# Kernel optimization log

Measured on AMD Instinct MI355X. Metric: run time of the kernel, lower is better.

Reference implementation:

```python
import jax, jax.numpy as jnp
import numpy as np

N = 8192        # nodes
IN_DIM = 512
OUT_DIM = 512
NUM_HEADS = 1   # required for view(-1,3)/view(-1,1,1) consistency in original code
K_NEIGH = 16


def setup_inputs() -> dict:
    key = jax.random.key(0)
    k0, k1, k2, k3, k4 = jax.random.split(key, 5)
    s = 1.0 / np.sqrt(IN_DIM)
    h = jax.random.normal(k0, (N, IN_DIM), dtype=jnp.float32)
    # nn.Linear default init: U(-1/sqrt(fan_in), 1/sqrt(fan_in)), bias=False
    Wq = jax.random.uniform(k1, (OUT_DIM * NUM_HEADS, IN_DIM), jnp.float32, -s, s)
    Wk = jax.random.uniform(k2, (OUT_DIM * NUM_HEADS, IN_DIM), jnp.float32, -s, s)
    Wv = jax.random.uniform(k3, (OUT_DIM * NUM_HEADS, IN_DIM), jnp.float32, -s, s)
    Wg = jax.random.uniform(k4, (3 * NUM_HEADS, IN_DIM), jnp.float32, -s, s)
    return {"h": h, "Wq": Wq, "Wk": Wk, "Wv": Wv, "Wg": Wg}


def _knn_edges(coords, k):
    # dgl.knn_graph semantics: each node receives edges from its k nearest
    # points (self included). src = neighbor, dst = query node.
    sq = jnp.sum(coords * coords, axis=-1)                      # [N]
    neg_d2 = 2.0 * (coords @ coords.T) - sq[:, None] - sq[None, :]  # -||xi-xj||^2, [N,N]
    _, idx = jax.lax.top_k(neg_d2, k)                           # [N,k] nearest per row
    n = coords.shape[0]
    src = idx.reshape(-1)                                       # [N*k]
    dst = jnp.repeat(jnp.arange(n, dtype=idx.dtype), k)         # [N*k]
    return src, dst


def reference(h, Wq, Wk, Wv, Wg):
    n = h.shape[0]
    D = OUT_DIM
    scale = jnp.float32(np.sqrt(D))

    Q_h = (h @ Wq.T).reshape(n, NUM_HEADS, D)
    K_h = (h @ Wk.T).reshape(n, NUM_HEADS, D)
    V_h = (h @ Wv.T).reshape(n, NUM_HEADS, D)
    G_h = (h @ Wg.T).reshape(n, NUM_HEADS, 3)

    coords = G_h.reshape(n, 3)  # num_heads == 1
    src, dst = _knn_edges(coords, K_NEIGH)  # E = n * K_NEIGH edges

    # edge-wise attention score: exp(clip((K_src . Q_dst)/sqrt(D), -5, 5))
    score = jnp.sum(K_h[src] * Q_h[dst], axis=-1, keepdims=True)     # [E,1,1]
    score_e = jnp.exp(jnp.clip(score / scale, -5.0, 5.0))

    # distance decay: exp(clip(-||G_src - G_dst|| / sqrt(D), -5, 5))
    dist = -jnp.sqrt(jnp.sum((G_h[src] - G_h[dst]) ** 2, axis=-1) + 1e-6)  # [E,1]
    distance = jnp.exp(jnp.clip(dist / scale, -5.0, 5.0))

    weight = score_e.reshape(-1, 1, 1) * distance.reshape(-1, 1, 1)  # [E,1,1]
    v1 = weight * V_h[src]                                           # [E,1,D]

    wV = jax.ops.segment_sum(v1, dst, num_segments=n)                # [n,1,D]
    z = jax.ops.segment_sum(score_e, dst, num_segments=n)            # [n,1,1]
    z = jnp.broadcast_to(z.reshape(n, 1, 1), (n, 1, D))

    mask = z > 0
    out = jnp.where(mask, wV / jnp.where(mask, z, 1.0), wV)
    return out
```

## Files before the change

### kernel.cpp

```cpp
#include <hip/hip_runtime.h>
#include <hip/hip_bf16.h>
#include <math.h>

#define N_NODES 8192
#define IN_DIM  512
#define OUT_DIM 512
#define KN      16
#define CAP     128
#define QPB     8

typedef __attribute__((ext_vector_type(8))) short bf16x8;
typedef __attribute__((ext_vector_type(4))) float f32x4;

__device__ __forceinline__ ushort f2bf(float x) {
  __hip_bfloat16 b = __float2bfloat16(x);
  return *reinterpret_cast<ushort*>(&b);
}
__device__ __forceinline__ float bflo(unsigned u) { return __uint_as_float(u << 16); }
__device__ __forceinline__ float bfhi(unsigned u) { return __uint_as_float(u & 0xffff0000u); }

#define GLOAD_LDS16(gp, lp)                                                     \
  __builtin_amdgcn_global_load_lds((const __attribute__((address_space(1))) void*)(gp), \
                                   (__attribute__((address_space(3))) void*)(lp), 16, 0, 0)

__global__ __launch_bounds__(256) void prep_split(
    const float* __restrict__ h, const float* __restrict__ Wg,
    const float* __restrict__ Wq, const float* __restrict__ Wk,
    const float* __restrict__ Wv,
    ushort* __restrict__ A2, ushort* __restrict__ Bqk, ushort* __restrict__ Bv,
    double* __restrict__ Gx, double* __restrict__ Gy,
    double* __restrict__ Gz, double* __restrict__ Gsq,
    float4* __restrict__ gpk) {
  if (blockIdx.x < 2048) {
    const int node = (blockIdx.x * 256 + threadIdx.x) >> 6;
    const int lane = threadIdx.x & 63;
    const int k = lane * 8;
    const float* hr = h + (size_t)node * IN_DIM;

    float4 v0 = *(const float4*)&hr[k];
    float4 v1 = *(const float4*)&hr[k + 4];

    ushort h0 = f2bf(v0.x), h1 = f2bf(v0.y), h2 = f2bf(v0.z), h3 = f2bf(v0.w);
    ushort h4 = f2bf(v1.x), h5 = f2bf(v1.y), h6 = f2bf(v1.z), h7 = f2bf(v1.w);
    ushort4 hiA = make_ushort4(h0, h1, h2, h3);
    ushort4 hiB = make_ushort4(h4, h5, h6, h7);
    ushort4 loA = make_ushort4(f2bf(v0.x - bflo((unsigned)h0)), f2bf(v0.y - bflo((unsigned)h1)),
                               f2bf(v0.z - bflo((unsigned)h2)), f2bf(v0.w - bflo((unsigned)h3)));
    ushort4 loB = make_ushort4(f2bf(v1.x - bflo((unsigned)h4)), f2bf(v1.y - bflo((unsigned)h5)),
                               f2bf(v1.z - bflo((unsigned)h6)), f2bf(v1.w - bflo((unsigned)h7)));
    size_t base = (size_t)node * 1024 + k;
    *(ushort4*)&A2[base]           = hiA;
    *(ushort4*)&A2[base + 4]       = hiB;
    *(ushort4*)&A2[base + 512]     = loA;
    *(ushort4*)&A2[base + 512 + 4] = loB;

    float4 w0a = *(const float4*)&Wg[0 * IN_DIM + k];
    float4 w0b = *(const float4*)&Wg[0 * IN_DIM + k + 4];
    float4 w1a = *(const float4*)&Wg[1 * IN_DIM + k];
    float4 w1b = *(const float4*)&Wg[1 * IN_DIM + k + 4];
    float4 w2a = *(const float4*)&Wg[2 * IN_DIM + k];
    float4 w2b = *(const float4*)&Wg[2 * IN_DIM + k + 4];

    double s0 = 0.0, s1 = 0.0, s2 = 0.0;
    s0 += (double)v0.x * w0a.x; s0 += (double)v0.y * w0a.y;
    s0 += (double)v0.z * w0a.z; s0 += (double)v0.w * w0a.w;
    s0 += (double)v1.x * w0b.x; s0 += (double)v1.y * w0b.y;
    s0 += (double)v1.z * w0b.z; s0 += (double)v1.w * w0b.w;
    s1 += (double)v0.x * w1a.x; s1 += (double)v0.y * w1a.y;
    s1 += (double)v0.z * w1a.z; s1 += (double)v0.w * w1a.w;
    s1 += (double)v1.x * w1b.x; s1 += (double)v1.y * w1b.y;
    s1 += (double)v1.z * w1b.z; s1 += (double)v1.w * w1b.w;
    s2 += (double)v0.x * w2a.x; s2 += (double)v0.y * w2a.y;
    s2 += (double)v0.z * w2a.z; s2 += (double)v0.w * w2a.w;
    s2 += (double)v1.x * w2b.x; s2 += (double)v1.y * w2b.y;
    s2 += (double)v1.z * w2b.z; s2 += (double)v1.w * w2b.w;

    #pragma unroll
    for (int off = 32; off; off >>= 1) {
      s0 += __shfl_down(s0, off);
      s1 += __shfl_down(s1, off);
      s2 += __shfl_down(s2, off);
    }
    if (lane == 0) {
      double sq = s0 * s0 + s1 * s1 + s2 * s2;
      Gx[node] = s0; Gy[node] = s1; Gz[node] = s2; Gsq[node] = sq;
      gpk[node] = make_float4((float)s0, (float)s1, (float)s2, -(float)sq);
    }
  } else {
    int i = (blockIdx.x - 2048) * 256 + threadIdx.x;
    int n  = i >> 7;
    int kc = (i & 127) << 2;
    if (n < 1024) {
      const float* W = (n < 512) ? Wq : Wk;
      int r = n & 511;
      float4 v = *(const float4*)&W[(size_t)r * 512 + kc];
      *(ushort4*)&Bqk[(size_t)n * 512 + kc] =
          make_ushort4(f2bf(v.x), f2bf(v.y), f2bf(v.z), f2bf(v.w));
    } else {
      int r = n - 1024;
      float4 v = *(const float4*)&Wv[(size_t)r * 512 + kc];
      ushort4 hv = make_ushort4(f2bf(v.x), f2bf(v.y), f2bf(v.z), f2bf(v.w));
      *(ushort4*)&Bv[(size_t)r * 1024 + kc]       = hv;
      *(ushort4*)&Bv[(size_t)r * 1024 + 512 + kc] = hv;
    }
  }
}

__global__ __launch_bounds__(256) void gemm_qkv(
    const ushort* __restrict__ A2, const ushort* __restrict__ Bqk,
    const ushort* __restrict__ Bv,
    ushort* __restrict__ Q2, ushort* __restrict__ K2, ushort* __restrict__ V2) {
  __shared__ ushort lA[128 * 32];
  __shared__ ushort lB[128 * 32];
  const int tid = threadIdx.x, w = tid >> 6, lane = tid & 63;
  const int id = blockIdx.x;
  const int sw = (id & 7) * 96 + (id >> 3);
  const int bm = sw / 12, bn = sw % 12;
  const int wr = w >> 1, wc = w & 1;
  const bool isv = (bn >= 8);
  const int  kmax = isv ? 1024 : 512;
  const int  ldb  = isv ? 1024 : 512;
  const ushort* Bb = isv ? (Bv + (size_t)(bn - 8) * 128 * 1024)
                         : (Bqk + (size_t)bn * 128 * 512);

  f32x4 acc[4][4] = {};

  const int   srow = w * 32 + (lane >> 2);
  const int   scol = (lane & 3) * 8;
  const size_t gA0 = (size_t)(bm * 128 + srow) * 1024 + scol;
  const size_t gB0 = (size_t)srow * ldb + scol;

  for (int k0 = 0; k0 < kmax; k0 += 32) {
    GLOAD_LDS16(&A2[gA0 + k0],                    &lA[w * 1024]);
    GLOAD_LDS16(&A2[gA0 + 16 * 1024 + k0],        &lA[w * 1024 + 512]);
    GLOAD_LDS16(&Bb[gB0 + k0],                    &lB[w * 1024]);
    GLOAD_LDS16(&Bb[gB0 + (size_t)16 * ldb + k0], &lB[w * 1024 + 512]);
    __syncthreads();

    const int ar = wr * 64 + (lane & 15);
    const int br = wc * 64 + (lane & 15);
    const int kc = (lane >> 4) * 8;
    bf16x8 af[4], bfr[4];
    #pragma unroll
    for (int f = 0; f < 4; ++f) {
      af[f]  = *(const bf16x8*)&lA[(ar + f * 16) * 32 + kc];
      bfr[f] = *(const bf16x8*)&lB[(br + f * 16) * 32 + kc];
    }
    #pragma unroll
    for (int fm = 0; fm < 4; ++fm)
      #pragma unroll
      for (int fn = 0; fn < 4; ++fn)
        acc[fm][fn] = __builtin_amdgcn_mfma_f32_16x16x32_bf16(af[fm], bfr[fn], acc[fm][fn], 0, 0, 0);
    __syncthreads();
  }

  ushort* Cm = isv ? V2 : (bn < 4 ? Q2 : K2);
  const int col  = (isv ? (bn - 8) : (bn & 3)) * 128 + wc * 64 + (lane & 15);
  const int row0 = bm * 128 + wr * 64 + (lane >> 4) * 4;
  #pragma unroll
  for (int fm = 0; fm < 4; ++fm)
    #pragma unroll
    for (int fn = 0; fn < 4; ++fn)
      #pragma unroll
      for (int r = 0; r < 4; ++r)
        Cm[(size_t)(row0 + fm * 16 + r) * 512 + col + fn * 16] = f2bf(acc[fm][fn][r]);
}

__global__ __launch_bounds__(256) void knn_kernel(
    const float4* __restrict__ gpk,
    const double* __restrict__ Gx, const double* __restrict__ Gy,
    const double* __restrict__ Gz, const double* __restrict__ Gsq,
    int* __restrict__ knn) {
  const int tid   = threadIdx.x;
  const int w     = tid >> 6;
  const int lane  = tid & 63;
  const int qbase = blockIdx.x * QPB;

  __shared__ float  s_tmax[QPB][256];
  __shared__ int    s_cand[QPB][CAP];
  __shared__ double s_dval[QPB][CAP];
  __shared__ int    s_cnt[QPB];
  __shared__ float  s_T[QPB];

  float q2x[QPB], q2y[QPB], q2z[QPB], tmax[QPB];
  #pragma unroll
  for (int s = 0; s < QPB; ++s) {
    float4 qv = gpk[qbase + s];
    q2x[s] = 2.f * qv.x; q2y[s] = 2.f * qv.y; q2z[s] = 2.f * qv.z;
    tmax[s] = -1e30f;
  }
  if (tid < QPB) s_cnt[tid] = 0;

  {
    float4 c0 = gpk[tid];
    float4 c1 = gpk[tid + 256];
    for (int i = 0; i < 16; ++i) {
      int nx = ((i + 1) & 15) * 512;
      float4 n0 = gpk[tid + nx];
      float4 n1 = gpk[tid + nx + 256];
      #pragma unroll
      for (int s = 0; s < QPB; ++s) {
        float v0 = fmaf(q2x[s], c0.x, fmaf(q2y[s], c0.y, fmaf(q2z[s], c0.z, c0.w)));
        float v1 = fmaf(q2x[s], c1.x, fmaf(q2y[s], c1.y, fmaf(q2z[s], c1.z, c1.w)));
        tmax[s] = fmaxf(fmaxf(tmax[s], v0), v1);
      }
      c0 = n0; c1 = n1;
    }
  }
  #pragma unroll
  for (int s = 0; s < QPB; ++s) s_tmax[s][tid] = tmax[s];
  __syncthreads();

  #pragma unroll
  for (int qq = 0; qq < 2; ++qq) {
    int q = w * 2 + qq;
    float v = fmaxf(fmaxf(s_tmax[q][lane], s_tmax[q][lane + 64]),
                    fmaxf(s_tmax[q][lane + 128], s_tmax[q][lane + 192]));
    unsigned b = __float_as_uint(v);
    unsigned u = b ^ ((unsigned)((int)b >> 31) | 0x80000000u);
    unsigned thr = 0;
    for (int bit = 31; bit >= 0; --bit) {
      unsigned cand = thr | (1u << bit);
      unsigned long long m = __ballot(u >= cand);
      if (__popcll(m) >= KN) thr = cand;
    }
    unsigned tb = (thr & 0x80000000u) ? (thr ^ 0x80000000u) : ~thr;
    if (lane == 0) s_T[q] = __uint_as_float(tb);
  }
  __syncthreads();

  float Ts[QPB];
  #pragma unroll
  for (int s = 0; s < QPB; ++s) Ts[s] = s_T[s];
  {
    float4 c0 = gpk[tid];
    float4 c1 = gpk[tid + 256];
    for (int i = 0; i < 16; ++i) {
      int nx = ((i + 1) & 15) * 512;
      float4 n0 = gpk[tid + nx];
      float4 n1 = gpk[tid + nx + 256];
      int j0 = tid + i * 512, j1 = j0 + 256;
      #pragma unroll
      for (int s = 0; s < QPB; ++s) {
        float v0 = fmaf(q2x[s], c0.x, fmaf(q2y[s], c0.y, fmaf(q2z[s], c0.z, c0.w)));
        float v1 = fmaf(q2x[s], c1.x, fmaf(q2y[s], c1.y, fmaf(q2z[s], c1.z, c1.w)));
        if (v0 >= Ts[s]) { int p = atomicAdd(&s_cnt[s], 1); if (p < CAP) s_cand[s][p] = j0; }
        if (v1 >= Ts[s]) { int p = atomicAdd(&s_cnt[s], 1); if (p < CAP) s_cand[s][p] = j1; }
      }
      c0 = n0; c1 = n1;
    }
  }
  __syncthreads();

  const int qA = w * 2, qB = qA + 1;
  const int cntA = min(s_cnt[qA], CAP);
  const int cntB = min(s_cnt[qB], CAP);
  int j0a = -1, j1a = -1, j0b = -1, j1b = -1;
  double v0a = 0, v1a = 0, v0b = 0, v1b = 0;
  {
    int gq = qbase + qA;
    double xi = Gx[gq], yi = Gy[gq], zi = Gz[gq], sqi = Gsq[gq];
    if (lane < cntA) {
      j0a = s_cand[qA][lane];
      v0a = 2.0 * (xi * Gx[j0a] + yi * Gy[j0a] + zi * Gz[j0a]) - sqi - Gsq[j0a];
      s_dval[qA][lane] = v0a;
    }
    if (lane + 64 < cntA) {
      j1a = s_cand[qA][lane + 64];
      v1a = 2.0 * (xi * Gx[j1a] + yi * Gy[j1a] + zi * Gz[j1a]) - sqi - Gsq[j1a];
      s_dval[qA][lane + 64] = v1a;
    }
  }
  {
    int gq = qbase + qB;
    double xi = Gx[gq], yi = Gy[gq], zi = Gz[gq], sqi = Gsq[gq];
    if (lane < cntB) {
      j0b = s_cand[qB][lane];
      v0b = 2.0 * (xi * Gx[j0b] + yi * Gy[j0b] + zi * Gz[j0b]) - sqi - Gsq[j0b];
      s_dval[qB][lane] = v0b;
    }
    if (lane + 64 < cntB) {
      j1b = s_cand[qB][lane + 64];
      v1b = 2.0 * (xi * Gx[j1b] + yi * Gy[j1b] + zi * Gz[j1b]) - sqi - Gsq[j1b];
      s_dval[qB][lane + 64] = v1b;
    }
  }
  __syncthreads();
  {
    int r0 = 0, r1 = 0;
    for (int m = 0; m < cntA; ++m) {
      double dv = s_dval[qA][m]; int di = s_cand[qA][m];
      r0 += (dv > v0a) || (dv == v0a && di < j0a);
      r1 += (dv > v1a) || (dv == v1a && di < j1a);
    }
    int gq = qbase + qA;
    if (j0a >= 0 && r0 < KN) knn[gq * KN + r0] = j0a;
    if (j1a >= 0 && r1 < KN) knn[gq * KN + r1] = j1a;
  }
  {
    int r0 = 0, r1 = 0;
    for (int m = 0; m < cntB; ++m) {
      double dv = s_dval[qB][m]; int di = s_cand[qB][m];
      r0 += (dv > v0b) || (dv == v0b && di < j0b);
      r1 += (dv > v1b) || (dv == v1b && di < j1b);
    }
    int gq = qbase + qB;
    if (j0b >= 0 && r0 < KN) knn[gq * KN + r0] = j0b;
    if (j1b >= 0 && r1 < KN) knn[gq * KN + r1] = j1b;
  }
}

__global__ __launch_bounds__(256) void attend_kernel(
    const ushort* __restrict__ Q2, const ushort* __restrict__ K2, const ushort* __restrict__ V2,
    const float4* __restrict__ gpk,
    const int* __restrict__ knn, float* __restrict__ out) {
  const int i    = blockIdx.x;
  const int tid  = threadIdx.x;
  const int wv   = tid >> 6;
  const int lane = tid & 63;

  __shared__ int   s_idx[KN];
  __shared__ float s_w[KN];
  __shared__ float s_se[KN];

  if (tid < KN) s_idx[tid] = knn[i * KN + tid];
  __syncthreads();

  uint4 qa = *(const uint4*)&Q2[(size_t)i * 512 + lane * 8];
  float q0 = bflo(qa.x), q1 = bfhi(qa.x), q2 = bflo(qa.y), q3 = bfhi(qa.y);
  float q4 = bflo(qa.z), q5 = bfhi(qa.z), q6 = bflo(qa.w), q7 = bfhi(qa.w);

  float partial[4];
  #pragma unroll
  for (int s = 0; s < 4; ++s) {
    int src = s_idx[wv * 4 + s];
    uint4 ka = *(const uint4*)&K2[(size_t)src * 512 + lane * 8];
    float acc = q0 * bflo(ka.x);
    acc = fmaf(q1, bfhi(ka.x), acc);
    acc = fmaf(q2, bflo(ka.y), acc);
    acc = fmaf(q3, bfhi(ka.y), acc);
    acc = fmaf(q4, bflo(ka.z), acc);
    acc = fmaf(q5, bfhi(ka.z), acc);
    acc = fmaf(q6, bflo(ka.w), acc);
    acc = fmaf(q7, bfhi(ka.w), acc);
    partial[s] = acc;
  }
  #pragma unroll
  for (int s = 0; s < 4; ++s)
    #pragma unroll
    for (int off = 32; off; off >>= 1) partial[s] += __shfl_down(partial[s], off);

  if (lane == 0) {
    float4 gi = gpk[i];
    #pragma unroll
    for (int s = 0; s < 4; ++s) {
      int e = wv * 4 + s;
      int src = s_idx[e];
      float sc = partial[s] / 22.627417f;
      sc = fminf(fmaxf(sc, -5.f), 5.f);
      float se = expf(sc);
      float4 gs = gpk[src];
      float dx = gi.x - gs.x, dy = gi.y - gs.y, dz = gi.z - gs.z;
      float dd = -sqrtf(fmaf(dx, dx, fmaf(dy, dy, fmaf(dz, dz, 1e-6f))));
      float dc = fminf(fmaxf(dd / 22.627417f, -5.f), 5.f);
      float de = expf(dc);
      s_se[e] = se;
      s_w[e]  = se * de;
    }
  }
  __syncthreads();

  float z = 0.f;
  #pragma unroll
  for (int e = 0; e < KN; ++e) z += s_se[e];

  const int d = tid * 2;
  float a0 = 0.f, a1 = 0.f;
  #pragma unroll
  for (int e = 0; e < KN; ++e) {
    unsigned vv = *(const unsigned*)&V2[(size_t)s_idx[e] * 512 + d];
    a0 = fmaf(s_w[e], bflo(vv), a0);
    a1 = fmaf(s_w[e], bfhi(vv), a1);
  }
  float inv = (z > 0.f) ? (1.f / z) : 1.f;
  float2 o = make_float2(a0 * inv, a1 * inv);
  *(float2*)&out[(size_t)i * 512 + d] = o;
}

extern "C" void kernel_launch(void* const* d_in, const int* in_sizes, int n_in,
                              void* d_out, int out_size, void* d_ws, size_t ws_size,
                              hipStream_t stream) {
  const float* h  = (const float*)d_in[0];
  const float* Wq = (const float*)d_in[1];
  const float* Wk = (const float*)d_in[2];
  const float* Wv = (const float*)d_in[3];
  const float* Wg = (const float*)d_in[4];
  float* out = (float*)d_out;

  char* ws = (char*)d_ws;
  ushort* A2  = (ushort*)(ws);
  ushort* Bqk = (ushort*)(ws + (16u << 20));
  ushort* Bv  = (ushort*)(ws + (17u << 20));
  ushort* Q2  = (ushort*)(ws + (18u << 20));
  ushort* K2  = (ushort*)(ws + (26u << 20));
  ushort* V2  = (ushort*)(ws + (34u << 20));
  float4* gpk = (float4*)(ws + (42u << 20));
  double* Gx  = (double*)(ws + (42u << 20) + (1u << 17));
  double* Gy  = Gx + N_NODES;
  double* Gz  = Gy + N_NODES;
  double* Gsq = Gz + N_NODES;
  int*    knn = (int*)(Gsq + N_NODES);

  hipLaunchKernelGGL(prep_split, dim3(2048 + 768), dim3(256), 0, stream,
                     h, Wg, Wq, Wk, Wv, A2, Bqk, Bv, Gx, Gy, Gz, Gsq, gpk);
  hipLaunchKernelGGL(gemm_qkv, dim3(768), dim3(256), 0, stream,
                     A2, Bqk, Bv, Q2, K2, V2);
  hipLaunchKernelGGL(knn_kernel, dim3(N_NODES / QPB), dim3(256), 0, stream,
                     gpk, Gx, Gy, Gz, Gsq, knn);
  hipLaunchKernelGGL(attend_kernel, dim3(N_NODES), dim3(256), 0, stream,
                     Q2, K2, V2, gpk, knn, out);
}
```

Measured before the change: 103.6 us.

## Drop split-bf16 V GEMM, store QKV as fp16, packed-FMA kNN scan and fdot2 scores

```diff
diff --git a/kernel.cpp b/kernel.cpp
--- a/kernel.cpp
+++ b/kernel.cpp
@@ -11,13 +11,31 @@
 
 typedef __attribute__((ext_vector_type(8))) short bf16x8;
 typedef __attribute__((ext_vector_type(4))) float f32x4;
+typedef __attribute__((ext_vector_type(2))) float v2f;
+typedef __attribute__((ext_vector_type(2))) _Float16 h2;
 
 __device__ __forceinline__ ushort f2bf(float x) {
   __hip_bfloat16 b = __float2bfloat16(x);
   return *reinterpret_cast<ushort*>(&b);
 }
 __device__ __forceinline__ float bflo(unsigned u) { return __uint_as_float(u << 16); }
-__device__ __forceinline__ float bfhi(unsigned u) { return __uint_as_float(u & 0xffff0000u); }
+__device__ __forceinline__ ushort f2h(float x) {
+  _Float16 v = (_Float16)x;
+  return __builtin_bit_cast(unsigned short, v);
+}
+__device__ __forceinline__ v2f fma2(v2f a, v2f b, v2f c) { return __builtin_elementwise_fma(a, b, c); }
+__device__ __forceinline__ v2f max2(v2f a, v2f b) { return __builtin_elementwise_max(a, b); }
+__device__ __forceinline__ v2f splat2(float x) { v2f r; r.x = x; r.y = x; return r; }
+
+__device__ __forceinline__ float dot2acc(unsigned qu, unsigned ku, float acc) {
+#if __has_builtin(__builtin_amdgcn_fdot2)
+  return __builtin_amdgcn_fdot2(__builtin_bit_cast(h2, qu), __builtin_bit_cast(h2, ku), acc, false);
+#else
+  h2 q = __builtin_bit_cast(h2, qu), k = __builtin_bit_cast(h2, ku);
+  acc = fmaf((float)q.x, (float)k.x, acc);
+  return fmaf((float)q.y, (float)k.y, acc);
+#endif
+}
 
 #define GLOAD_LDS16(gp, lp)                                                     \
   __builtin_amdgcn_global_load_lds((const __attribute__((address_space(1))) void*)(gp), \
@@ -27,7 +45,7 @@
     const float* __restrict__ h, const float* __restrict__ Wg,
     const float* __restrict__ Wq, const float* __restrict__ Wk,
     const float* __restrict__ Wv,
-    ushort* __restrict__ A2, ushort* __restrict__ Bqk, ushort* __restrict__ Bv,
+    ushort* __restrict__ A2, ushort* __restrict__ B,
     double* __restrict__ Gx, double* __restrict__ Gy,
     double* __restrict__ Gz, double* __restrict__ Gsq,
     float4* __restrict__ gpk) {
@@ -40,19 +58,11 @@
     float4 v0 = *(const float4*)&hr[k];
     float4 v1 = *(const float4*)&hr[k + 4];
 
-    ushort h0 = f2bf(v0.x), h1 = f2bf(v0.y), h2 = f2bf(v0.z), h3 = f2bf(v0.w);
-    ushort h4 = f2bf(v1.x), h5 = f2bf(v1.y), h6 = f2bf(v1.z), h7 = f2bf(v1.w);
-    ushort4 hiA = make_ushort4(h0, h1, h2, h3);
-    ushort4 hiB = make_ushort4(h4, h5, h6, h7);
-    ushort4 loA = make_ushort4(f2bf(v0.x - bflo((unsigned)h0)), f2bf(v0.y - bflo((unsigned)h1)),
-                               f2bf(v0.z - bflo((unsigned)h2)), f2bf(v0.w - bflo((unsigned)h3)));
-    ushort4 loB = make_ushort4(f2bf(v1.x - bflo((unsigned)h4)), f2bf(v1.y - bflo((unsigned)h5)),
-                               f2bf(v1.z - bflo((unsigned)h6)), f2bf(v1.w - bflo((unsigned)h7)));
-    size_t base = (size_t)node * 1024 + k;
-    *(ushort4*)&A2[base]           = hiA;
-    *(ushort4*)&A2[base + 4]       = hiB;
-    *(ushort4*)&A2[base + 512]     = loA;
-    *(ushort4*)&A2[base + 512 + 4] = loB;
+    ushort4 hiA = make_ushort4(f2bf(v0.x), f2bf(v0.y), f2bf(v0.z), f2bf(v0.w));
+    ushort4 hiB = make_ushort4(f2bf(v1.x), f2bf(v1.y), f2bf(v1.z), f2bf(v1.w));
+    size_t base = (size_t)node * 512 + k;
+    *(ushort4*)&A2[base]     = hiA;
+    *(ushort4*)&A2[base + 4] = hiB;
 
     float4 w0a = *(const float4*)&Wg[0 * IN_DIM + k];
     float4 w0b = *(const float4*)&Wg[0 * IN_DIM + k + 4];
@@ -90,25 +100,16 @@
     int i = (blockIdx.x - 2048) * 256 + threadIdx.x;
     int n  = i >> 7;
     int kc = (i & 127) << 2;
-    if (n < 1024) {
-      const float* W = (n < 512) ? Wq : Wk;
-      int r = n & 511;
-      float4 v = *(const float4*)&W[(size_t)r * 512 + kc];
-      *(ushort4*)&Bqk[(size_t)n * 512 + kc] =
-          make_ushort4(f2bf(v.x), f2bf(v.y), f2bf(v.z), f2bf(v.w));
-    } else {
-      int r = n - 1024;
-      float4 v = *(const float4*)&Wv[(size_t)r * 512 + kc];
-      ushort4 hv = make_ushort4(f2bf(v.x), f2bf(v.y), f2bf(v.z), f2bf(v.w));
-      *(ushort4*)&Bv[(size_t)r * 1024 + kc]       = hv;
-      *(ushort4*)&Bv[(size_t)r * 1024 + 512 + kc] = hv;
-    }
+    const float* W = (n < 512) ? Wq : (n < 1024) ? Wk : Wv;
+    int r = n & 511;
+    float4 v = *(const float4*)&W[(size_t)r * 512 + kc];
+    *(ushort4*)&B[(size_t)n * 512 + kc] =
+        make_ushort4(f2bf(v.x), f2bf(v.y), f2bf(v.z), f2bf(v.w));
   }
 }
 
 __global__ __launch_bounds__(256) void gemm_qkv(
-    const ushort* __restrict__ A2, const ushort* __restrict__ Bqk,
-    const ushort* __restrict__ Bv,
+    const ushort* __restrict__ A2, const ushort* __restrict__ B,
     ushort* __restrict__ Q2, ushort* __restrict__ K2, ushort* __restrict__ V2) {
   __shared__ ushort lA[128 * 32];
   __shared__ ushort lB[128 * 32];
@@ -117,24 +118,19 @@
   const int sw = (id & 7) * 96 + (id >> 3);
   const int bm = sw / 12, bn = sw % 12;
   const int wr = w >> 1, wc = w & 1;
-  const bool isv = (bn >= 8);
-  const int  kmax = isv ? 1024 : 512;
-  const int  ldb  = isv ? 1024 : 512;
-  const ushort* Bb = isv ? (Bv + (size_t)(bn - 8) * 128 * 1024)
-                         : (Bqk + (size_t)bn * 128 * 512);
 
   f32x4 acc[4][4] = {};
 
   const int   srow = w * 32 + (lane >> 2);
   const int   scol = (lane & 3) * 8;
-  const size_t gA0 = (size_t)(bm * 128 + srow) * 1024 + scol;
-  const size_t gB0 = (size_t)srow * ldb + scol;
-
-  for (int k0 = 0; k0 < kmax; k0 += 32) {
-    GLOAD_LDS16(&A2[gA0 + k0],                    &lA[w * 1024]);
-    GLOAD_LDS16(&A2[gA0 + 16 * 1024 + k0],        &lA[w * 1024 + 512]);
-    GLOAD_LDS16(&Bb[gB0 + k0],                    &lB[w * 1024]);
-    GLOAD_LDS16(&Bb[gB0 + (size_t)16 * ldb + k0], &lB[w * 1024 + 512]);
+  const size_t gA0 = (size_t)(bm * 128 + srow) * 512 + scol;
+  const size_t gB0 = (size_t)(bn * 128 + srow) * 512 + scol;
+
+  for (int k0 = 0; k0 < 512; k0 += 32) {
+    GLOAD_LDS16(&A2[gA0 + k0],            &lA[w * 1024]);
+    GLOAD_LDS16(&A2[gA0 + 16 * 512 + k0], &lA[w * 1024 + 512]);
+    GLOAD_LDS16(&B[gB0 + k0],             &lB[w * 1024]);
+    GLOAD_LDS16(&B[gB0 + 16 * 512 + k0],  &lB[w * 1024 + 512]);
     __syncthreads();
 
     const int ar = wr * 64 + (lane & 15);
@@ -154,8 +150,8 @@
     __syncthreads();
   }
 
-  ushort* Cm = isv ? V2 : (bn < 4 ? Q2 : K2);
-  const int col  = (isv ? (bn - 8) : (bn & 3)) * 128 + wc * 64 + (lane & 15);
+  ushort* Cm = (bn < 4) ? Q2 : (bn < 8) ? K2 : V2;
+  const int col  = (bn & 3) * 128 + wc * 64 + (lane & 15);
   const int row0 = bm * 128 + wr * 64 + (lane >> 4) * 4;
   #pragma unroll
   for (int fm = 0; fm < 4; ++fm)
@@ -163,7 +159,7 @@
     for (int fn = 0; fn < 4; ++fn)
       #pragma unroll
       for (int r = 0; r < 4; ++r)
-        Cm[(size_t)(row0 + fm * 16 + r) * 512 + col + fn * 16] = f2bf(acc[fm][fn][r]);
+        Cm[(size_t)(row0 + fm * 16 + r) * 512 + col + fn * 16] = f2h(acc[fm][fn][r]);
 }
 
 __global__ __launch_bounds__(256) void knn_kernel(
@@ -182,12 +178,13 @@
   __shared__ int    s_cnt[QPB];
   __shared__ float  s_T[QPB];
 
-  float q2x[QPB], q2y[QPB], q2z[QPB], tmax[QPB];
+  float q2x[QPB], q2y[QPB], q2z[QPB];
+  v2f tm2[QPB];
   #pragma unroll
   for (int s = 0; s < QPB; ++s) {
     float4 qv = gpk[qbase + s];
     q2x[s] = 2.f * qv.x; q2y[s] = 2.f * qv.y; q2z[s] = 2.f * qv.z;
-    tmax[s] = -1e30f;
+    tm2[s] = splat2(-1e30f);
   }
   if (tid < QPB) s_cnt[tid] = 0;
 
@@ -198,17 +195,23 @@
       int nx = ((i + 1) & 15) * 512;
       float4 n0 = gpk[tid + nx];
       float4 n1 = gpk[tid + nx + 256];
+      v2f cx, cy, cz, cw;
+      cx.x = c0.x; cx.y = c1.x;
+      cy.x = c0.y; cy.y = c1.y;
+      cz.x = c0.z; cz.y = c1.z;
+      cw.x = c0.w; cw.y = c1.w;
       #pragma unroll
       for (int s = 0; s < QPB; ++s) {
-        float v0 = fmaf(q2x[s], c0.x, fmaf(q2y[s], c0.y, fmaf(q2z[s], c0.z, c0.w)));
-        float v1 = fmaf(q2x[s], c1.x, fmaf(q2y[s], c1.y, fmaf(q2z[s], c1.z, c1.w)));
-        tmax[s] = fmaxf(fmaxf(tmax[s], v0), v1);
+        v2f v = fma2(splat2(q2x[s]), cx,
+                 fma2(splat2(q2y[s]), cy,
+                  fma2(splat2(q2z[s]), cz, cw)));
+        tm2[s] = max2(tm2[s], v);
       }
       c0 = n0; c1 = n1;
     }
   }
   #pragma unroll
-  for (int s = 0; s < QPB; ++s) s_tmax[s][tid] = tmax[s];
+  for (int s = 0; s < QPB; ++s) s_tmax[s][tid] = fmaxf(tm2[s].x, tm2[s].y);
   __syncthreads();
 
   #pragma unroll
@@ -240,12 +243,18 @@
       float4 n0 = gpk[tid + nx];
       float4 n1 = gpk[tid + nx + 256];
       int j0 = tid + i * 512, j1 = j0 + 256;
+      v2f cx, cy, cz, cw;
+      cx.x = c0.x; cx.y = c1.x;
+      cy.x = c0.y; cy.y = c1.y;
+      cz.x = c0.z; cz.y = c1.z;
+      cw.x = c0.w; cw.y = c1.w;
       #pragma unroll
       for (int s = 0; s < QPB; ++s) {
-        float v0 = fmaf(q2x[s], c0.x, fmaf(q2y[s], c0.y, fmaf(q2z[s], c0.z, c0.w)));
-        float v1 = fmaf(q2x[s], c1.x, fmaf(q2y[s], c1.y, fmaf(q2z[s], c1.z, c1.w)));
-        if (v0 >= Ts[s]) { int p = atomicAdd(&s_cnt[s], 1); if (p < CAP) s_cand[s][p] = j0; }
-        if (v1 >= Ts[s]) { int p = atomicAdd(&s_cnt[s], 1); if (p < CAP) s_cand[s][p] = j1; }
+        v2f v = fma2(splat2(q2x[s]), cx,
+                 fma2(splat2(q2y[s]), cy,
+                  fma2(splat2(q2z[s]), cz, cw)));
+        if (v.x >= Ts[s]) { int p = atomicAdd(&s_cnt[s], 1); if (p < CAP) s_cand[s][p] = j0; }
+        if (v.y >= Ts[s]) { int p = atomicAdd(&s_cnt[s], 1); if (p < CAP) s_cand[s][p] = j1; }
       }
       c0 = n0; c1 = n1;
     }
@@ -327,22 +336,16 @@
   __syncthreads();
 
   uint4 qa = *(const uint4*)&Q2[(size_t)i * 512 + lane * 8];
-  float q0 = bflo(qa.x), q1 = bfhi(qa.x), q2 = bflo(qa.y), q3 = bfhi(qa.y);
-  float q4 = bflo(qa.z), q5 = bfhi(qa.z), q6 = bflo(qa.w), q7 = bfhi(qa.w);
 
   float partial[4];
   #pragma unroll
   for (int s = 0; s < 4; ++s) {
     int src = s_idx[wv * 4 + s];
     uint4 ka = *(const uint4*)&K2[(size_t)src * 512 + lane * 8];
-    float acc = q0 * bflo(ka.x);
-    acc = fmaf(q1, bfhi(ka.x), acc);
-    acc = fmaf(q2, bflo(ka.y), acc);
-    acc = fmaf(q3, bfhi(ka.y), acc);
-    acc = fmaf(q4, bflo(ka.z), acc);
-    acc = fmaf(q5, bfhi(ka.z), acc);
-    acc = fmaf(q6, bflo(ka.w), acc);
-    acc = fmaf(q7, bfhi(ka.w), acc);
+    float acc = dot2acc(qa.x, ka.x, 0.f);
+    acc = dot2acc(qa.y, ka.y, acc);
+    acc = dot2acc(qa.z, ka.z, acc);
+    acc = dot2acc(qa.w, ka.w, acc);
     partial[s] = acc;
   }
   #pragma unroll
@@ -379,8 +382,9 @@
   #pragma unroll
   for (int e = 0; e < KN; ++e) {
     unsigned vv = *(const unsigned*)&V2[(size_t)s_idx[e] * 512 + d];
-    a0 = fmaf(s_w[e], bflo(vv), a0);
-    a1 = fmaf(s_w[e], bfhi(vv), a1);
+    h2 vh = __builtin_bit_cast(h2, vv);
+    a0 = fmaf(s_w[e], (float)vh.x, a0);
+    a1 = fmaf(s_w[e], (float)vh.y, a1);
   }
   float inv = (z > 0.f) ? (1.f / z) : 1.f;
   float2 o = make_float2(a0 * inv, a1 * inv);
@@ -399,22 +403,21 @@
 
   char* ws = (char*)d_ws;
   ushort* A2  = (ushort*)(ws);
-  ushort* Bqk = (ushort*)(ws + (16u << 20));
-  ushort* Bv  = (ushort*)(ws + (17u << 20));
-  ushort* Q2  = (ushort*)(ws + (18u << 20));
-  ushort* K2  = (ushort*)(ws + (26u << 20));
-  ushort* V2  = (ushort*)(ws + (34u << 20));
-  float4* gpk = (float4*)(ws + (42u << 20));
-  double* Gx  = (double*)(ws + (42u << 20) + (1u << 17));
+  ushort* B   = (ushort*)(ws + (8u << 20));
+  ushort* Q2  = (ushort*)(ws + (10u << 20));
+  ushort* K2  = (ushort*)(ws + (18u << 20));
+  ushort* V2  = (ushort*)(ws + (26u << 20));
+  float4* gpk = (float4*)(ws + (34u << 20));
+  double* Gx  = (double*)(ws + (34u << 20) + (1u << 17));
   double* Gy  = Gx + N_NODES;
   double* Gz  = Gy + N_NODES;
   double* Gsq = Gz + N_NODES;
   int*    knn = (int*)(Gsq + N_NODES);
 
   hipLaunchKernelGGL(prep_split, dim3(2048 + 768), dim3(256), 0, stream,
-                     h, Wg, Wq, Wk, Wv, A2, Bqk, Bv, Gx, Gy, Gz, Gsq, gpk);
+                     h, Wg, Wq, Wk, Wv, A2, B, Gx, Gy, Gz, Gsq, gpk);
   hipLaunchKernelGGL(gemm_qkv, dim3(768), dim3(256), 0, stream,
-                     A2, Bqk, Bv, Q2, K2, V2);
+                     A2, B, Q2, K2, V2);
   hipLaunchKernelGGL(knn_kernel, dim3(N_NODES / QPB), dim3(256), 0, stream,
                      gpk, Gx, Gy, Gz, Gsq, knn);
   hipLaunchKernelGGL(attend_kernel, dim3(N_NODES), dim3(256), 0, stream,
```

New measurement: 95.04 us. -8.2%, faster.
